# Kernel tuning notes

Hardware: AMD Instinct MI355X
Metric: run time of the kernel (lower is better)

The kernel has to match this reference:

```python
import jax, jax.numpy as jnp
import numpy as np

B_GRAPHS = 256
N_PER = 512
N = B_GRAPHS * N_PER            # 131072 nodes
E = 1048576                     # edges (avg degree 8)
H = 64                          # hidden_dim
L = 3                           # num_layers
R = 128                         # rnn_dim
NODE_IN = 2
EDGE_IN = 2
OUT = 2
JK = L * H


def setup_inputs() -> dict:
    key = jax.random.key(0)
    ks = jax.random.split(key, 40)
    # intra-graph random edges
    g = jax.random.randint(ks[0], (E,), 0, B_GRAPHS)
    src = g * N_PER + jax.random.randint(ks[1], (E,), 0, N_PER)
    dst = g * N_PER + jax.random.randint(ks[2], (E,), 0, N_PER)
    edge_index = jnp.stack([src, dst]).astype(jnp.int64)
    batch = jnp.repeat(jnp.arange(B_GRAPHS, dtype=jnp.int64), N_PER)

    p = lambda k, shp: jax.random.normal(k, shp, jnp.float32) * 0.1
    return dict(
        x=jax.random.normal(ks[3], (N, NODE_IN), jnp.float32),
        edge_attr=jax.random.normal(ks[4], (E, EDGE_IN), jnp.float32),
        node_W=p(ks[5], (NODE_IN, H)), node_b=p(ks[6], (H,)),
        edgeemb_W=p(ks[7], (EDGE_IN, H)), edgeemb_b=p(ks[8], (H,)),
        gat_W=p(ks[9], (L, H, H)), gat_Wedge=p(ks[10], (L, H, H)),
        gat_att_src=p(ks[11], (L, H)), gat_att_dst=p(ks[12], (L, H)),
        gat_att_edge=p(ks[13], (L, H)), gat_b=p(ks[14], (L, H)),
        gru_wih_f=p(ks[15], (3 * R, JK)), gru_whh_f=p(ks[16], (3 * R, R)),
        gru_bih_f=p(ks[17], (3 * R,)), gru_bhh_f=p(ks[18], (3 * R,)),
        gru_wih_b=p(ks[19], (3 * R, JK)), gru_whh_b=p(ks[20], (3 * R, R)),
        gru_bih_b=p(ks[21], (3 * R,)), gru_bhh_b=p(ks[22], (3 * R,)),
        head_W1=p(ks[23], (2 * R, 64)), head_b1=p(ks[24], (64,)),
        head_W2=p(ks[25], (64, OUT)), head_b2=p(ks[26], (OUT,)),
        edge_index=edge_index, batch=batch,
    )


def _gru_dir(xs, wih, whh, bih, bhh):
    # xs: [T, B, F] -> outputs [T, B, R]  (PyTorch GRU cell equations)
    gx = xs @ wih.T + bih  # precompute input gates [T, B, 3R]
    h0 = jnp.zeros((xs.shape[1], R), xs.dtype)

    def step(h, g):
        gh = h @ whh.T + bhh
        r = jax.nn.sigmoid(g[..., :R] + gh[..., :R])
        z = jax.nn.sigmoid(g[..., R:2 * R] + gh[..., R:2 * R])
        n = jnp.tanh(g[..., 2 * R:] + r * gh[..., 2 * R:])
        hn = (1.0 - z) * n + z * h
        return hn, hn

    _, ys = jax.lax.scan(step, h0, gx)
    return ys


def _forward(x, edge_attr, node_W, node_b, edgeemb_W, edgeemb_b,
             gat_W, gat_Wedge, gat_att_src, gat_att_dst, gat_att_edge, gat_b,
             gru_wih_f, gru_whh_f, gru_bih_f, gru_bhh_f,
             gru_wih_b, gru_whh_b, gru_bih_b, gru_bhh_b,
             head_W1, head_b1, head_W2, head_b2, edge_index, batch):
    src, dst = edge_index[0], edge_index[1]
    h = x @ node_W + node_b                     # [N, H]
    e = edge_attr @ edgeemb_W + edgeemb_b       # [E, H]

    # PyG GATConv default add_self_loops=True, fill_value='mean':
    # self-loop edge feature = mean of incoming edge features per node
    ones = jnp.ones((E,), e.dtype)
    deg = jax.ops.segment_sum(ones, dst, num_segments=N)
    e_loop = jax.ops.segment_sum(e, dst, num_segments=N) / jnp.maximum(deg, 1.0)[:, None]
    ar = jnp.arange(N, dtype=src.dtype)
    srcF = jnp.concatenate([src, ar])
    dstF = jnp.concatenate([dst, ar])
    eF = jnp.concatenate([e, e_loop], axis=0)   # [E+N, H]

    outs = []
    for l in range(L):
        xp = h @ gat_W[l]                                   # [N, H]
        a_s = xp @ gat_att_src[l]                           # [N]
        a_d = xp @ gat_att_dst[l]                           # [N]
        a_e = (eF @ gat_Wedge[l]) @ gat_att_edge[l]         # [E+N]
        alpha = jax.nn.leaky_relu(a_s[srcF] + a_d[dstF] + a_e, 0.2)
        m = jax.ops.segment_max(alpha, dstF, num_segments=N)
        ex = jnp.exp(alpha - m[dstF])
        den = jax.ops.segment_sum(ex, dstF, num_segments=N)
        w = ex / den[dstF]                                  # segment softmax
        agg = jax.ops.segment_sum(w[:, None] * xp[srcF], dstF, num_segments=N) + gat_b[l]
        h = jax.nn.leaky_relu(agg, 0.01)                    # F.leaky_relu default slope
        outs.append(h)

    h_jk = jnp.concatenate(outs, axis=-1)                   # [N, JK]
    # to_dense_batch: sorted equal-size graphs -> dense reshape, mask all True
    dense = h_jk.reshape(B_GRAPHS, N_PER, JK)
    xs = dense.transpose(1, 0, 2)                           # [T, B, JK]
    yf = _gru_dir(xs, gru_wih_f, gru_whh_f, gru_bih_f, gru_bhh_f)
    yb = _gru_dir(xs[::-1], gru_wih_b, gru_whh_b, gru_bih_b, gru_bhh_b)[::-1]
    rnn_out = jnp.concatenate([yf, yb], axis=-1).transpose(1, 0, 2)  # [B, T, 2R]
    out = jax.nn.relu(rnn_out @ head_W1 + head_b1) @ head_W2 + head_b2
    return out.reshape(N, OUT)                              # out[mask], mask full


def reference(x, edge_attr, node_W, node_b, edgeemb_W, edgeemb_b,
              gat_W, gat_Wedge, gat_att_src, gat_att_dst, gat_att_edge, gat_b,
              gru_wih_f, gru_whh_f, gru_bih_f, gru_bhh_f,
              gru_wih_b, gru_whh_b, gru_bih_b, gru_bhh_b,
              head_W1, head_b1, head_W2, head_b2, edge_index, batch):
    return _forward(x, edge_attr, node_W, node_b, edgeemb_W, edgeemb_b,
                    gat_W, gat_Wedge, gat_att_src, gat_att_dst, gat_att_edge, gat_b,
                    gru_wih_f, gru_whh_f, gru_bih_f, gru_bhh_f,
                    gru_wih_b, gru_whh_b, gru_bih_b, gru_bhh_b,
                    head_W1, head_b1, head_W2, head_b2, edge_index, batch)
```

## Files before the change

### kernel.cpp

```cpp
#include <hip/hip_runtime.h>
#include <cstdint>
#include <cstddef>

typedef _Float16 half_t;
typedef _Float16 half8 __attribute__((ext_vector_type(8)));
typedef float f32x4 __attribute__((ext_vector_type(4)));

constexpr int NN = 131072;
constexpr int NE = 1048576;
constexpr int NPER = 512;

#define DEVINL __device__ __forceinline__

DEVINL float sigm_(float x){ float e = __expf(-x); return __builtin_amdgcn_rcpf(1.f+e); }
DEVINL float tanh_(float x){
  x = fminf(15.f, fmaxf(-15.f, x));
  float e = __expf(-2.f*x);
  return (1.f-e)*__builtin_amdgcn_rcpf(1.f+e);
}

#define LDS_BARRIER() asm volatile("s_waitcnt lgkmcnt(0)\ns_barrier" ::: "memory")


__global__ void const_kernel(const float* __restrict__ gatWe,
                             const float* __restrict__ attE, const float* __restrict__ eW,
                             const float* __restrict__ eb, float* __restrict__ cc){
  int l = blockIdx.x, k = threadIdx.x;
  const float* Wel = gatWe + l*4096;
  float s3=0.f;
  for (int j=0;j<64;j++) s3 += Wel[k*64+j]*attE[l*64+j];
  float c0 = eW[k]*s3, c1 = eW[64+k]*s3, cb = eb[k]*s3;
  for (int off=1; off<64; off<<=1){
    c0 += __shfl_xor(c0,off); c1 += __shfl_xor(c1,off); cb += __shfl_xor(cb,off);
  }
  if (k==0){ cc[l]=c0; cc[3+l]=c1; cc[6+l]=cb; }
}

__global__ void prep_pack(const float* __restrict__ wih_f, const float* __restrict__ wih_b,
                          const float* __restrict__ head_W1, const float* __restrict__ gat_W,
                          const float* __restrict__ bih_f, const float* __restrict__ bih_b,
                          const float* __restrict__ whh_f, const float* __restrict__ whh_b,
                          half_t* __restrict__ BcombT, half_t* __restrict__ W1T,
                          half_t* __restrict__ BTgat, float* __restrict__ bias_comb,
                          half_t* __restrict__ whh16){
  int gid = blockIdx.x*256 + threadIdx.x;
  if (gid < 147456){
    int j = gid/192, k = gid%192;
    float v = (j<384)? wih_f[j*192+k] : wih_b[(j-384)*192+k];
    BcombT[gid] = (half_t)v;
  } else if (gid < 163840){
    int i = gid - 147456;
    int n = i>>8, k = i&255;
    W1T[i] = (half_t)head_W1[k*64+n];
  } else if (gid < 176128){
    int i = gid - 163840;
    int l = i>>12, r = i&4095;
    int n = r>>6, k = r&63;
    BTgat[i] = (half_t)gat_W[l*4096 + k*64 + n];
  } else if (gid < 176896){
    int i = gid - 176128;
    int j = (i<384)? i : i-384;
    bias_comb[i] = (i<384)? bih_f[j] : bih_b[j];
  } else if (gid < 275200){
    int i = gid - 176896;
    float v = (i<49152)? whh_f[i] : whh_b[i-49152];
    whh16[i] = (half_t)v;
  }
}

__global__ void bias_fold(const float* __restrict__ bhh_f, const float* __restrict__ bhh_b,
                          float* __restrict__ bias_comb){
  int i = threadIdx.x + blockIdx.x*256;
  if (i < 256)      bias_comb[i]       += bhh_f[i];
  else if (i < 512) bias_comb[i+128]   += bhh_b[i-256];
}

__global__ __launch_bounds__(256) void embed_kernel(const float* __restrict__ x,
                            const float* __restrict__ nW, const float* __restrict__ nb,
                            half_t* __restrict__ h){
  int gid = blockIdx.x*256 + threadIdx.x;
  int n = gid>>6, j = gid&63;
  float v = x[2*n]*nW[j] + x[2*n+1]*nW[64+j] + nb[j];
  h[(size_t)n*64+j] = (half_t)v;
}

__global__ __launch_bounds__(256) void deg_count(const int* __restrict__ ei,
                          int* __restrict__ deg, int* __restrict__ tmp){
  int e = blockIdx.x*256 + threadIdx.x;
  int dt = ei[NE+e];
  tmp[e] = atomicAdd(&deg[dt],1);
}

__global__ __launch_bounds__(256) void scan1(const int* __restrict__ deg, int* __restrict__ rowstart,
                      int* __restrict__ bsum){
  __shared__ int sc[256];
  int b=blockIdx.x, t=threadIdx.x, i=b*256+t;
  int v=deg[i]; sc[t]=v; __syncthreads();
  for (int off=1; off<256; off<<=1){
    int tv = (t>=off)? sc[t-off] : 0;
    __syncthreads(); sc[t]+=tv; __syncthreads();
  }
  rowstart[i]=sc[t]-v;
  if (t==255) bsum[b]=sc[255];
}
__global__ void scan2(int* __restrict__ bsum){
  __shared__ int sc[512];
  int t=threadIdx.x; int v=bsum[t]; sc[t]=v; __syncthreads();
  for (int off=1; off<512; off<<=1){
    int tv = (t>=off)? sc[t-off] : 0;
    __syncthreads(); sc[t]+=tv; __syncthreads();
  }
  bsum[t]=sc[t]-v;
}
__global__ __launch_bounds__(256) void scan3(int* __restrict__ rowstart, const int* __restrict__ bsum){
  int b=blockIdx.x, t=threadIdx.x, i=b*256+t;
  rowstart[i]+=bsum[b];
}

__global__ __launch_bounds__(256) void fill2(const int* __restrict__ ei, const float* __restrict__ ea,
                      const int* __restrict__ rowstart, const int* __restrict__ tmp,
                      int4* __restrict__ rec){
  int e = blockIdx.x*256 + threadIdx.x;
  int dt = ei[NE+e];
  int slot = rowstart[dt] + tmp[e];
  int4 r;
  r.x = ei[e];
  r.y = __float_as_int(ea[2*e]);
  r.z = __float_as_int(ea[2*e+1]);
  r.w = dt;
  rec[slot] = r;
}

__global__ __launch_bounds__(256) void means_kernel(const int* __restrict__ deg, const int* __restrict__ rowstart,
                         const int4* __restrict__ rec, float2* __restrict__ m01){
  int n = blockIdx.x*256 + threadIdx.x;
  int st = rowstart[n], cnt = deg[n];
  float s0=0.f, s1=0.f;
  for (int i=0;i<cnt;i++){
    int4 r = rec[st+i];
    s0 += __int_as_float(r.y);
    s1 += __int_as_float(r.z);
  }
  float inv = 1.f/(float)max(cnt,1);
  float2 m; m.x = s0*inv; m.y = s1*inv;
  m01[n] = m;
}

__global__ __launch_bounds__(256) void gemm_xp(const half_t* __restrict__ A, int lda,
                        const half_t* __restrict__ BT,
                        const float* __restrict__ attS, const float* __restrict__ attD,
                        half_t* __restrict__ xp, float* __restrict__ a_s, float* __restrict__ a_d){
  __shared__ half_t As[128*32];
  __shared__ half_t Bs[64*32];
  const int tid = threadIdx.x, m0 = blockIdx.x*128;
  const int w = tid>>6, lane = tid&63;
  const int lm = lane&15, quad = lane>>4;
  const int wm0 = w*32;
  f32x4 acc[2][4] = {};
  for (int k0=0;k0<64;k0+=32){
    {
      const int c0 = tid*2;
      #pragma unroll
      for (int u=0;u<2;u++){
        int c=c0+u; int row=c>>2; int off=(c&3)*8;
        *(half8*)(&As[row*32+off]) = *(const half8*)(&A[(size_t)(m0+row)*lda + k0 + off]);
      }
      int c=tid; int row=c>>2; int off=(c&3)*8;
      *(half8*)(&Bs[row*32+off]) = *(const half8*)(&BT[(size_t)row*64 + k0 + off]);
    }
    __syncthreads();
    half8 af[2], bf[4];
    #pragma unroll
    for (int nt=0;nt<4;nt++) bf[nt] = *(const half8*)(&Bs[(nt*16+lm)*32 + quad*8]);
    #pragma unroll
    for (int mt=0;mt<2;mt++) af[mt] = *(const half8*)(&As[(wm0+mt*16+lm)*32 + quad*8]);
    #pragma unroll
    for (int mt=0;mt<2;mt++)
      #pragma unroll
      for (int nt=0;nt<4;nt++)
        acc[mt][nt] = __builtin_amdgcn_mfma_f32_16x16x32_f16(af[mt], bf[nt], acc[mt][nt], 0,0,0);
    __syncthreads();
  }
  float vsv[4], vdv[4];
  #pragma unroll
  for (int nt=0;nt<4;nt++){ vsv[nt]=attS[nt*16+lm]; vdv[nt]=attD[nt*16+lm]; }
  #pragma unroll
  for (int mt=0;mt<2;mt++)
   #pragma unroll
   for (int r=0;r<4;r++){
    int m = m0+wm0+mt*16+quad*4+r;
    float ps=0.f, pd=0.f;
    #pragma unroll
    for (int nt=0;nt<4;nt++){
      float v = acc[mt][nt][r];
      xp[(size_t)m*64 + nt*16+lm] = (half_t)v;
      ps += v*vsv[nt]; pd += v*vdv[nt];
    }
    ps += __shfl_xor(ps,1); ps += __shfl_xor(ps,2); ps += __shfl_xor(ps,4); ps += __shfl_xor(ps,8);
    pd += __shfl_xor(pd,1); pd += __shfl_xor(pd,2); pd += __shfl_xor(pd,4); pd += __shfl_xor(pd,8);
    if (lm==0){ a_s[m]=ps; a_d[m]=pd; }
  }
}

__global__ __launch_bounds__(256) void edge_w(const int4* __restrict__ rec,
                       const float* __restrict__ a_s, const float* __restrict__ a_d,
                       const float* __restrict__ cc, int l, int2* __restrict__ sw,
                       const int* __restrict__ deg, const float2* __restrict__ m01,
                       float* __restrict__ wsf){
  int b = blockIdx.x;
  if (b < 4096){
    int s = b*256 + threadIdx.x;
    int4 r = rec[s];
    float al = a_s[r.x] + a_d[r.w]
             + __int_as_float(r.y)*cc[l] + __int_as_float(r.z)*cc[3+l] + cc[6+l];
    al = al>0.f? al : 0.2f*al;
    int2 o; o.x = r.x; o.y = __float_as_int(__expf(al));
    sw[s] = o;
  } else {
    int n = (b-4096)*256 + threadIdx.x;
    int cnt = deg[n];
    float2 m = m01[n];
    float ael = cnt? (m.x*cc[l] + m.y*cc[3+l] + cc[6+l]) : 0.f;
    float asl = a_s[n] + a_d[n] + ael;
    asl = asl>0.f? asl : 0.2f*asl;
    wsf[n] = __expf(asl);
  }
}

constexpr int SWCAP = 1536;
__global__ __launch_bounds__(512,4) void agg_lds(const int* __restrict__ rowstart, const int* __restrict__ deg,
                          const int2* __restrict__ sw, const float* __restrict__ wsf, int l,
                          const half_t* __restrict__ xp, const float* __restrict__ bias,
                          half_t* __restrict__ hjk){
  __shared__ half_t xs[512*64];
  __shared__ int2  swl[SWCAP];
  __shared__ int   nst[128];
  __shared__ int   ncnt[128];
  __shared__ float nwsf[128];
  const int g = blockIdx.x >> 2;
  const int sub = blockIdx.x & 3;
  const int tid = threadIdx.x;
  const int nbase = g*512 + sub*128;
  const int segst = rowstart[nbase];
  const int segend = rowstart[nbase+127] + deg[nbase+127];
  const int segcnt = segend - segst;
  {
    const half8* srcp = (const half8*)(xp + (size_t)g*32768);
    half8* dstp = (half8*)xs;
    #pragma unroll
    for (int i=0;i<8;i++)
      dstp[tid + i*512] = srcp[tid + i*512];
    int scap = segcnt < SWCAP ? segcnt : SWCAP;
    for (int i=tid; i<scap; i+=512)
      swl[i] = sw[segst+i];
    if (tid < 128){
      int n = nbase + tid;
      nst[tid]  = rowstart[n] - segst;
      ncnt[tid] = deg[n];
      nwsf[tid] = wsf[n];
    }
  }
  __syncthreads();
  const int w = tid>>6, lane = tid&63;
  const float bv = bias[lane];
  const int nb2 = nbase + w*16;
  for (int i=0;i<16;i++){
    const int li = w*16 + i;
    int st = nst[li], cnt = ncnt[li];
    float acc=0.f, den=0.f;
    if (cnt>0){
      if (st + cnt <= SWCAP){
        int q = cnt>>2, rem = cnt&3;
        int L0=q+(rem>0), L1=q+(rem>1), L2=q+(rem>2), L3=q;
        int s1v=L0, s2v=L0+L1, s3v=s2v+L2;
        int2 p0={0,0},p1={0,0},p2={0,0},p3={0,0};
        float x0v=0.f,x1v=0.f,x2v=0.f,x3v=0.f;
        if (L0>0){ p0=swl[st];     x0v=(float)xs[(p0.x&511)*64+lane]; }
        if (L1>0){ p1=swl[st+s1v]; x1v=(float)xs[(p1.x&511)*64+lane]; }
        if (L2>0){ p2=swl[st+s2v]; x2v=(float)xs[(p2.x&511)*64+lane]; }
        if (L3>0){ p3=swl[st+s3v]; x3v=(float)xs[(p3.x&511)*64+lane]; }
        for (int k=0;k<L0;k++){
          int2 n0=p0,n1=p1,n2=p2,n3=p3;
          float y0=0.f,y1=0.f,y2=0.f,y3=0.f;
          if (k+1<L0){ n0=swl[st+k+1];     y0=(float)xs[(n0.x&511)*64+lane]; }
          if (k+1<L1){ n1=swl[st+s1v+k+1]; y1=(float)xs[(n1.x&511)*64+lane]; }
          if (k+1<L2){ n2=swl[st+s2v+k+1]; y2=(float)xs[(n2.x&511)*64+lane]; }
          if (k+1<L3){ n3=swl[st+s3v+k+1]; y3=(float)xs[(n3.x&511)*64+lane]; }
          { float ww=__int_as_float(p0.y); den+=ww; acc+=ww*x0v; }
          if (k<L1){ float ww=__int_as_float(p1.y); den+=ww; acc+=ww*x1v; }
          if (k<L2){ float ww=__int_as_float(p2.y); den+=ww; acc+=ww*x2v; }
          if (k<L3){ float ww=__int_as_float(p3.y); den+=ww; acc+=ww*x3v; }
          p0=n0;p1=n1;p2=n2;p3=n3;
          x0v=y0;x1v=y1;x2v=y2;x3v=y3;
        }
      } else {
        int2 p = sw[segst+st];
        float xv = (float)xs[(p.x&511)*64 + lane];
        for (int k=0;k<cnt;k++){
          int2 pn = p; float xvn=0.f;
          if (k+1<cnt){
            pn = sw[segst+st+k+1];
            xvn = (float)xs[(pn.x&511)*64 + lane];
          }
          float ww = __int_as_float(p.y);
          den += ww;
          acc += ww*xv;
          p = pn; xv = xvn;
        }
      }
    }
    float wsfv = nwsf[li];
    den += wsfv;
    acc += wsfv*(float)xs[((nb2+i)&511)*64 + lane];
    float v = acc/den + bv;
    v = v>0.f? v : 0.01f*v;
    hjk[(size_t)(nb2+i)*192 + l*64 + lane] = (half_t)v;
  }
}

__global__ __launch_bounds__(256) void gemm_head(const half_t* __restrict__ A,
                        const half_t* __restrict__ W1T, const float* __restrict__ b1,
                        const float* __restrict__ W2, const float* __restrict__ b2,
                        float* __restrict__ out){
  __shared__ half_t As[128*32];
  __shared__ half_t Bs[64*32];
  const int tid = threadIdx.x, m0 = blockIdx.x*128;
  const int w = tid>>6, lane = tid&63;
  const int lm = lane&15, quad = lane>>4;
  const int wm0 = w*32;
  f32x4 acc[2][4] = {};
  for (int k0=0;k0<256;k0+=32){
    {
      const int c0 = tid*2;
      #pragma unroll
      for (int u=0;u<2;u++){
        int c=c0+u; int row=c>>2; int off=(c&3)*8;
        *(half8*)(&As[row*32+off]) = *(const half8*)(&A[(size_t)(m0+row)*256 + k0 + off]);
      }
      int c=tid; int row=c>>2; int off=(c&3)*8;
      *(half8*)(&Bs[row*32+off]) = *(const half8*)(&W1T[(size_t)row*256 + k0 + off]);
    }
    __syncthreads();
    half8 af[2], bf[4];
    #pragma unroll
    for (int nt=0;nt<4;nt++) bf[nt] = *(const half8*)(&Bs[(nt*16+lm)*32 + quad*8]);
    #pragma unroll
    for (int mt=0;mt<2;mt++) af[mt] = *(const half8*)(&As[(wm0+mt*16+lm)*32 + quad*8]);
    #pragma unroll
    for (int mt=0;mt<2;mt++)
      #pragma unroll
      for (int nt=0;nt<4;nt++)
        acc[mt][nt] = __builtin_amdgcn_mfma_f32_16x16x32_f16(af[mt], bf[nt], acc[mt][nt], 0,0,0);
    __syncthreads();
  }
  float b1v[4], w20[4], w21[4];
  #pragma unroll
  for (int nt=0;nt<4;nt++){
    int n = nt*16+lm;
    b1v[nt]=b1[n]; w20[nt]=W2[n*2]; w21[nt]=W2[n*2+1];
  }
  float b20=b2[0], b21=b2[1];
  #pragma unroll
  for (int mt=0;mt<2;mt++)
   #pragma unroll
   for (int r=0;r<4;r++){
    int m = m0+wm0+mt*16+quad*4+r;
    float p0=0.f, p1=0.f;
    #pragma unroll
    for (int nt=0;nt<4;nt++){
      float v = acc[mt][nt][r] + b1v[nt];
      v = v>0.f? v : 0.f;
      p0 += v*w20[nt]; p1 += v*w21[nt];
    }
    p0 += __shfl_xor(p0,1); p0 += __shfl_xor(p0,2); p0 += __shfl_xor(p0,4); p0 += __shfl_xor(p0,8);
    p1 += __shfl_xor(p1,1); p1 += __shfl_xor(p1,2); p1 += __shfl_xor(p1,4); p1 += __shfl_xor(p1,8);
    if (lm==0){
      out[(size_t)m*2]   = p0 + b20;
      out[(size_t)m*2+1] = p1 + b21;
    }
  }
}

__global__ __launch_bounds__(512,1) void gru_fused(
    const half_t* __restrict__ whh16, const float* __restrict__ bhh_f, const float* __restrict__ bhh_b,
    const half_t* __restrict__ gxf, const half_t* __restrict__ gxb,
    float* __restrict__ hstate, half_t* __restrict__ y, int c, int gruBlocks,
    const half_t* __restrict__ hjk, const half_t* __restrict__ BcombT, const float* __restrict__ biasc,
    half_t* __restrict__ gxf_n, half_t* __restrict__ gxb_n, int s0f, int s0b){
  __shared__ __align__(16) char SMEM[16384];
  const int bid = blockIdx.x;
  const int tid = threadIdx.x;
  if (bid < gruBlocks){
    __builtin_amdgcn_s_setprio(1);
    auto& H = *(half_t (*)[2][16][132])SMEM;
    half_t* slab0 = (half_t*)(SMEM + 8448);
    half_t* slab1 = (half_t*)(SMEM + 8448 + 3072);

    const int d = bid >> 6, gblk = bid & 63;
    const half_t* __restrict__ gx = d ? gxb : gxf;
    const float* bhh = d ? bhh_b : bhh_f;
    const int w = tid >> 6, lane = tid & 63;
    const int l15 = lane & 15, quad = lane >> 4;
    const int unit = w*16 + l15;

    half8 bf[3][4];
    float bhn = bhh[256 + unit];
    {
      const half_t* wbase = whh16 + (size_t)d*49152;
      #pragma unroll
      for (int g=0; g<3; g++){
        const half_t* wp = wbase + (size_t)(g*128 + unit)*128;
        #pragma unroll
        for (int kk=0; kk<4; kk++)
          bf[g][kk] = *(const half8*)(wp + kk*32 + quad*8);
      }
    }

    float hreg = hstate[((size_t)d*256 + gblk*4 + quad)*128 + unit];

    const bool loader = (w >= 4 && w < 7);
    const int jsl = d ? -384 : 384;
    int idx8 = 0;
    const half_t* srcp = nullptr;
    if (loader){
      int idx = (w-4)*64 + lane;
      int g_loc = idx/48, o = idx - g_loc*48;
      idx8 = idx*8;
      int j0 = d ? 127 : 0;
      srcp = gx + ((size_t)(gblk*4 + g_loc)*128 + j0)*384 + o*8;
    }

    const int cgg = tid >> 6;
    const int cpart = (tid & 63)*2;
    const int pos0 = d ? (511 - c*128) : (c*128);
    const int ystep = d ? -256 : 256;
    half_t* yptr = y + ((size_t)(gblk*4 + cgg)*512 + pos0)*256 + d*128 + cpart;

    for (int i=tid; i<2112; i+=512) ((uint*)SMEM)[i] = 0;
    LDS_BARRIER();
    H[0][quad*4][unit] = (half_t)hreg;
    half8 lvA, lvB;
    if (loader){
      lvA = *(const half8*)srcp; srcp += jsl;
      *(half8*)(slab0 + idx8) = lvA;
      lvB = *(const half8*)srcp; srcp += jsl;
    }
    LDS_BARRIER();

    auto stepf = [&](const half_t* cs, half_t* ns, int rd, int wr2,
                     half8& lvI, half8& lvW, bool pfi, bool pfw, bool cp){
      if (loader && pfi){ lvI = *(const half8*)srcp; srcp += jsl; }
      if (cp && tid < 256){
        uint hv = *(const uint*)&H[rd][cgg*4][cpart];
        *(uint*)yptr = hv;
        yptr += ystep;
      }
      float g0 = (float)cs[quad*384 + unit];
      float g1 = (float)cs[quad*384 + 128 + unit];
      float g2 = (float)cs[quad*384 + 256 + unit];
      half8 af[4] = {};
      if ((l15 & 3) == 0){
        #pragma unroll
        for (int kk=0; kk<4; kk++)
          af[kk] = *(const half8*)&H[rd][l15][kk*32 + quad*8];
      }
      f32x4 P[3] = {};
      #pragma unroll
      for (int kk=0; kk<4; kk++)
        #pragma unroll
        for (int g=0; g<3; g++)
          P[g] = __builtin_amdgcn_mfma_f32_16x16x32_f16(af[kk], bf[g][kk], P[g], 0,0,0);
      float rr = sigm_(g0 + P[0][0]);
      float zz = sigm_(g1 + P[1][0]);
      float nn = tanh_(g2 + rr*(P[2][0] + bhn));
      float hn = nn + zz*(hreg - nn);
      hreg = hn;
      H[wr2][quad*4][unit] = (half_t)hn;
      if (loader && pfw) *(half8*)(ns + idx8) = lvW;
      LDS_BARRIER();
    };

    stepf(slab0, slab1, 0,1, lvA, lvB, true,  true,  false);
    stepf(slab1, slab0, 1,0, lvB, lvA, true,  true,  true);
    for (int it=1; it<63; it++){
      stepf(slab0, slab1, 0,1, lvA, lvB, true, true, true);
      stepf(slab1, slab0, 1,0, lvB, lvA, true, true, true);
    }
    stepf(slab0, slab1, 0,1, lvA, lvB, false, true,  true);
    stepf(slab1, slab0, 1,0, lvB, lvA, false, false, true);
    if (tid < 256){
      uint hv = *(const uint*)&H[0][cgg*4][cpart];
      *(uint*)yptr = hv;
    }
    __builtin_amdgcn_s_setprio(0);
    hstate[((size_t)d*256 + gblk*4 + quad)*128 + unit] = hreg;
  } else {
    half_t* As = (half_t*)SMEM;
    half_t* Bs = (half_t*)(SMEM + 8192);
    const int gb = bid - gruBlocks;
    const int bx = gb & 255, by = gb >> 8;
    const int m0 = bx*128;
    const bool back = by >= 3;
    const int n0 = (back ? by-3 : by)*128;
    const int step0 = back ? s0b : s0f;
    half_t* C = back ? gxb_n : gxf_n;
    const half_t* BTh = BcombT + (back ? (size_t)384*192 : 0);
    const float* bh = biasc + (back ? 384 : 0);
    const int w = tid>>6, lane = tid&63;
    const int lm = lane&15, quad = lane>>4;
    const int wm0 = (w>>2)*64, wn0 = (w&3)*32;
    f32x4 acc[4][2] = {};
    for (int k0=0; k0<192; k0+=32){
      {
        int cidx = tid; int row = cidx>>2; int off = (cidx&3)*8;
        int m = m0+row;
        size_t arow = (size_t)(m>>7)*512 + step0 + (m&127);
        *(half8*)(&As[row*32+off]) = *(const half8*)(&hjk[arow*192 + k0 + off]);
        *(half8*)(&Bs[row*32+off]) = *(const half8*)(&BTh[(size_t)(n0+row)*192 + k0 + off]);
      }
      __syncthreads();
      half8 af[4], bfr[2];
      #pragma unroll
      for (int nt=0;nt<2;nt++) bfr[nt] = *(const half8*)(&Bs[(wn0+nt*16+lm)*32 + quad*8]);
      #pragma unroll
      for (int mt=0;mt<4;mt++) af[mt] = *(const half8*)(&As[(wm0+mt*16+lm)*32 + quad*8]);
      #pragma unroll
      for (int mt=0;mt<4;mt++)
        #pragma unroll
        for (int nt=0;nt<2;nt++)
          acc[mt][nt] = __builtin_amdgcn_mfma_f32_16x16x32_f16(af[mt], bfr[nt], acc[mt][nt], 0,0,0);
      __syncthreads();
    }
    #pragma unroll
    for (int mt=0;mt<4;mt++)
     #pragma unroll
     for (int nt=0;nt<2;nt++)
      #pragma unroll
      for (int r=0;r<4;r++){
        int m = m0+wm0+mt*16+quad*4+r;
        int n = n0+wn0+nt*16+lm;
        float v = acc[mt][nt][r] + bh[n];
        C[(size_t)m*384 + n] = (half_t)v;
      }
  }
}

extern "C" void kernel_launch(void* const* d_in, const int* in_sizes, int n_in,
                              void* d_out, int out_size, void* d_ws, size_t ws_size,
                              hipStream_t stream) {
  const float* x       = (const float*)d_in[0];
  const float* ea      = (const float*)d_in[1];
  const float* node_W  = (const float*)d_in[2];
  const float* node_b  = (const float*)d_in[3];
  const float* eW      = (const float*)d_in[4];
  const float* eb      = (const float*)d_in[5];
  const float* gat_W   = (const float*)d_in[6];
  const float* gat_We  = (const float*)d_in[7];
  const float* attS    = (const float*)d_in[8];
  const float* attD    = (const float*)d_in[9];
  const float* attE    = (const float*)d_in[10];
  const float* gat_b   = (const float*)d_in[11];
  const float* wih_f   = (const float*)d_in[12];
  const float* whh_f   = (const float*)d_in[13];
  const float* bih_f   = (const float*)d_in[14];
  const float* bhh_f   = (const float*)d_in[15];
  const float* wih_b   = (const float*)d_in[16];
  const float* whh_b   = (const float*)d_in[17];
  const float* bih_b   = (const float*)d_in[18];
  const float* bhh_b   = (const float*)d_in[19];
  const float* head_W1 = (const float*)d_in[20];
  const float* head_b1 = (const float*)d_in[21];
  const float* head_W2 = (const float*)d_in[22];
  const float* head_b2 = (const float*)d_in[23];
  const int*   ei      = (const int*)d_in[24];
  float* out = (float*)d_out;
  char* ws = (char*)d_ws;
  (void)in_sizes; (void)n_in; (void)out_size; (void)ws_size;

  size_t o = 0;
  auto alloc = [&](size_t bytes)->size_t{ size_t r=o; o += (bytes+255)&~(size_t)255; return r; };
  size_t o_cc     = alloc(16*4);
  size_t o_biasc  = alloc(768*4);
  size_t o_BcombT = alloc((size_t)768*192*2);
  size_t o_BTgat  = alloc((size_t)3*4096*2);
  size_t o_W1T    = alloc((size_t)64*256*2);
  size_t o_whh16  = alloc((size_t)2*49152*2);
  size_t o_hstate = alloc((size_t)2*256*128*4);
  size_t shared_base = o;

  size_t o_deg    = alloc((size_t)NN*4);
  size_t zero_end = o;
  size_t o_tmp    = alloc((size_t)NE*4);
  size_t o_rows   = alloc((size_t)NN*4);
  size_t o_bsum   = alloc(512*4);
  size_t o_rec    = alloc((size_t)NE*16);
  size_t o_sw     = alloc((size_t)NE*8);
  size_t o_m01    = alloc((size_t)NN*8);
  size_t o_as     = alloc((size_t)NN*4);
  size_t o_ad     = alloc((size_t)NN*4);
  size_t o_wsf    = alloc((size_t)NN*4);
  size_t o_h      = alloc((size_t)NN*64*2);
  size_t o_xp     = alloc((size_t)NN*64*2);
  size_t gat_end  = o;
  size_t gat_size = gat_end - shared_base;

  const size_t GXC    = (size_t)256*128*384*2;
  const size_t HJK_SZ = (size_t)NN*192*2;
  size_t shared_sz = gat_size > 4*GXC ? gat_size : 4*GXC;
  size_t o_gx0f = shared_base;
  size_t o_gx0b = shared_base + GXC;
  size_t o_gx1f = shared_base + 2*GXC;
  size_t o_gx1b = shared_base + 3*GXC;
  size_t o_hjk = shared_base + shared_sz;
  size_t o_y   = o_hjk + HJK_SZ;

  int*    deg    = (int*)(ws+o_deg);
  int*    tmp    = (int*)(ws+o_tmp);
  int*    rows   = (int*)(ws+o_rows);
  int*    bsum   = (int*)(ws+o_bsum);
  int4*   rec    = (int4*)(ws+o_rec);
  int2*   sw     = (int2*)(ws+o_sw);
  float2* m01    = (float2*)(ws+o_m01);
  float*  a_s    = (float*)(ws+o_as);
  float*  a_d    = (float*)(ws+o_ad);
  float*  wsf    = (float*)(ws+o_wsf);
  float*  cc     = (float*)(ws+o_cc);
  float*  biasc  = (float*)(ws+o_biasc);
  half_t* h      = (half_t*)(ws+o_h);
  half_t* xp     = (half_t*)(ws+o_xp);
  half_t* hjk    = (half_t*)(ws+o_hjk);
  half_t* BcombT = (half_t*)(ws+o_BcombT);
  half_t* BTgat  = (half_t*)(ws+o_BTgat);
  half_t* W1T    = (half_t*)(ws+o_W1T);
  half_t* whh16  = (half_t*)(ws+o_whh16);
  float*  hstate = (float*)(ws+o_hstate);
  half_t* gxbuf[2][2] = {{(half_t*)(ws+o_gx0f), (half_t*)(ws+o_gx0b)},
                         {(half_t*)(ws+o_gx1f), (half_t*)(ws+o_gx1b)}};
  half_t* y      = (half_t*)(ws+o_y);

  hipMemsetAsync(ws+shared_base, 0, zero_end-shared_base, stream);
  hipMemsetAsync(ws+o_hstate, 0, (size_t)2*256*128*4, stream);

  const_kernel<<<3,64,0,stream>>>(gat_We, attE, eW, eb, cc);
  prep_pack<<<1075,256,0,stream>>>(wih_f, wih_b, head_W1, gat_W, bih_f, bih_b, whh_f, whh_b,
                                   BcombT, W1T, BTgat, biasc, whh16);
  bias_fold<<<2,256,0,stream>>>(bhh_f, bhh_b, biasc);
  embed_kernel<<<32768,256,0,stream>>>(x, node_W, node_b, h);
  deg_count<<<4096,256,0,stream>>>(ei, deg, tmp);
  scan1<<<512,256,0,stream>>>(deg, rows, bsum);
  scan2<<<1,512,0,stream>>>(bsum);
  scan3<<<512,256,0,stream>>>(rows, bsum);
  fill2<<<4096,256,0,stream>>>(ei, ea, rows, tmp, rec);
  means_kernel<<<512,256,0,stream>>>(deg, rows, rec, m01);

  for (int l=0;l<3;l++){
    const half_t* in = (l==0)? h : (hjk + (size_t)(l-1)*64);
    int lda = (l==0)? 64 : 192;
    gemm_xp<<<1024,256,0,stream>>>(in, lda, BTgat + (size_t)l*4096, attS + l*64, attD + l*64, xp, a_s, a_d);
    edge_w<<<4608,256,0,stream>>>(rec, a_s, a_d, cc, l, sw, deg, m01, wsf);
    agg_lds<<<1024,512,0,stream>>>(rows, deg, sw, wsf, l, xp, gat_b + l*64, hjk);
  }

  gru_fused<<<1536,512,0,stream>>>(whh16, bhh_f, bhh_b, gxbuf[0][0], gxbuf[0][1], hstate, y, 0, 0,
                                   hjk, BcombT, biasc, gxbuf[0][0], gxbuf[0][1], 0, 384);
  for (int c=0;c<4;c++){
    int buf = c&1, nbuf = (c+1)&1;
    int grid = 128 + (c<3 ? 1536 : 0);
    gru_fused<<<grid,512,0,stream>>>(whh16, bhh_f, bhh_b, gxbuf[buf][0], gxbuf[buf][1], hstate, y, c, 128,
                                     hjk, BcombT, biasc, gxbuf[nbuf][0], gxbuf[nbuf][1],
                                     (c+1)*128, (2-c)*128);
  }

  gemm_head<<<1024,256,0,stream>>>(y, W1T, head_b1, head_W2, head_b2, out);
}
```

Before: 770.8 us.

## Aggregate GAT messages via LDS atomics instead of per-node gather from staged features

```diff
diff --git a/kernel.cpp b/kernel.cpp
--- a/kernel.cpp
+++ b/kernel.cpp
@@ -214,7 +214,9 @@
     float al = a_s[r.x] + a_d[r.w]
              + __int_as_float(r.y)*cc[l] + __int_as_float(r.z)*cc[3+l] + cc[6+l];
     al = al>0.f? al : 0.2f*al;
-    int2 o; o.x = r.x; o.y = __float_as_int(__expf(al));
+    int2 o;
+    o.x = (r.x & 511) | ((r.w & 127) << 16);
+    o.y = __float_as_int(__expf(al));
     sw[s] = o;
   } else {
     int n = (b-4096)*256 + threadIdx.x;
@@ -232,89 +234,57 @@
                           const int2* __restrict__ sw, const float* __restrict__ wsf, int l,
                           const half_t* __restrict__ xp, const float* __restrict__ bias,
                           half_t* __restrict__ hjk){
-  __shared__ half_t xs[512*64];
   __shared__ int2  swl[SWCAP];
-  __shared__ int   nst[128];
-  __shared__ int   ncnt[128];
-  __shared__ float nwsf[128];
-  const int g = blockIdx.x >> 2;
-  const int sub = blockIdx.x & 3;
+  __shared__ float accl[128*64];
+  __shared__ float denl[128];
   const int tid = threadIdx.x;
-  const int nbase = g*512 + sub*128;
+  const int nbase = blockIdx.x*128;
+  const half_t* __restrict__ xpg = xp + ((size_t)(nbase >> 9))*32768;
   const int segst = rowstart[nbase];
   const int segend = rowstart[nbase+127] + deg[nbase+127];
   const int segcnt = segend - segst;
-  {
-    const half8* srcp = (const half8*)(xp + (size_t)g*32768);
-    half8* dstp = (half8*)xs;
-    #pragma unroll
-    for (int i=0;i<8;i++)
-      dstp[tid + i*512] = srcp[tid + i*512];
-    int scap = segcnt < SWCAP ? segcnt : SWCAP;
-    for (int i=tid; i<scap; i+=512)
-      swl[i] = sw[segst+i];
-    if (tid < 128){
-      int n = nbase + tid;
-      nst[tid]  = rowstart[n] - segst;
-      ncnt[tid] = deg[n];
-      nwsf[tid] = wsf[n];
-    }
-  }
+  const int w = tid>>6, lane = tid&63;
+  #pragma unroll
+  for (int i=0;i<16;i++) accl[tid + i*512] = 0.f;
+  if (tid < 128) denl[tid] = 0.f;
+  int scap = segcnt < SWCAP ? segcnt : SWCAP;
+  for (int i=tid; i<scap; i+=512) swl[i] = sw[segst+i];
+  int e0 = rowstart[nbase + w*16] - segst;
+  int e1 = (w==7) ? segcnt : (rowstart[nbase + w*16 + 16] - segst);
   __syncthreads();
-  const int w = tid>>6, lane = tid&63;
+  if (segcnt <= SWCAP){
+    for (int e=e0; e<e1; ++e){
+      int2 p = swl[e];
+      int dl   = p.x >> 16;
+      int srcl = p.x & 511;
+      float xv = (float)xpg[(size_t)srcl*64 + lane];
+      float ww = __int_as_float(p.y);
+      atomicAdd(&accl[dl*64 + lane], ww*xv);
+      if (lane == 0) atomicAdd(&denl[dl], ww);
+    }
+  } else {
+    for (int e=e0; e<e1; ++e){
+      int2 p = sw[segst + e];
+      int dl   = p.x >> 16;
+      int srcl = p.x & 511;
+      float xv = (float)xpg[(size_t)srcl*64 + lane];
+      float ww = __int_as_float(p.y);
+      atomicAdd(&accl[dl*64 + lane], ww*xv);
+      if (lane == 0) atomicAdd(&denl[dl], ww);
+    }
+  }
+  __syncthreads();
   const float bv = bias[lane];
-  const int nb2 = nbase + w*16;
+  #pragma unroll
   for (int i=0;i<16;i++){
-    const int li = w*16 + i;
-    int st = nst[li], cnt = ncnt[li];
-    float acc=0.f, den=0.f;
-    if (cnt>0){
-      if (st + cnt <= SWCAP){
-        int q = cnt>>2, rem = cnt&3;
-        int L0=q+(rem>0), L1=q+(rem>1), L2=q+(rem>2), L3=q;
-        int s1v=L0, s2v=L0+L1, s3v=s2v+L2;
-        int2 p0={0,0},p1={0,0},p2={0,0},p3={0,0};
-        float x0v=0.f,x1v=0.f,x2v=0.f,x3v=0.f;
-        if (L0>0){ p0=swl[st];     x0v=(float)xs[(p0.x&511)*64+lane]; }
-        if (L1>0){ p1=swl[st+s1v]; x1v=(float)xs[(p1.x&511)*64+lane]; }
-        if (L2>0){ p2=swl[st+s2v]; x2v=(float)xs[(p2.x&511)*64+lane]; }
-        if (L3>0){ p3=swl[st+s3v]; x3v=(float)xs[(p3.x&511)*64+lane]; }
-        for (int k=0;k<L0;k++){
-          int2 n0=p0,n1=p1,n2=p2,n3=p3;
-          float y0=0.f,y1=0.f,y2=0.f,y3=0.f;
-          if (k+1<L0){ n0=swl[st+k+1];     y0=(float)xs[(n0.x&511)*64+lane]; }
-          if (k+1<L1){ n1=swl[st+s1v+k+1]; y1=(float)xs[(n1.x&511)*64+lane]; }
-          if (k+1<L2){ n2=swl[st+s2v+k+1]; y2=(float)xs[(n2.x&511)*64+lane]; }
-          if (k+1<L3){ n3=swl[st+s3v+k+1]; y3=(float)xs[(n3.x&511)*64+lane]; }
-          { float ww=__int_as_float(p0.y); den+=ww; acc+=ww*x0v; }
-          if (k<L1){ float ww=__int_as_float(p1.y); den+=ww; acc+=ww*x1v; }
-          if (k<L2){ float ww=__int_as_float(p2.y); den+=ww; acc+=ww*x2v; }
-          if (k<L3){ float ww=__int_as_float(p3.y); den+=ww; acc+=ww*x3v; }
-          p0=n0;p1=n1;p2=n2;p3=n3;
-          x0v=y0;x1v=y1;x2v=y2;x3v=y3;
-        }
-      } else {
-        int2 p = sw[segst+st];
-        float xv = (float)xs[(p.x&511)*64 + lane];
-        for (int k=0;k<cnt;k++){
-          int2 pn = p; float xvn=0.f;
-          if (k+1<cnt){
-            pn = sw[segst+st+k+1];
-            xvn = (float)xs[(pn.x&511)*64 + lane];
-          }
-          float ww = __int_as_float(p.y);
-          den += ww;
-          acc += ww*xv;
-          p = pn; xv = xvn;
-        }
-      }
-    }
-    float wsfv = nwsf[li];
-    den += wsfv;
-    acc += wsfv*(float)xs[((nb2+i)&511)*64 + lane];
-    float v = acc/den + bv;
+    int li = w*16 + i;
+    float accv = accl[li*64 + lane];
+    float den  = denl[li];
+    float wsfv = wsf[nbase + li];
+    float xv   = (float)xpg[(size_t)(((nbase+li)&511))*64 + lane];
+    float v = (accv + wsfv*xv)/(den + wsfv) + bv;
     v = v>0.f? v : 0.01f*v;
-    hjk[(size_t)(nb2+i)*192 + l*64 + lane] = (half_t)v;
+    hjk[(size_t)(nbase+li)*192 + l*64 + lane] = (half_t)v;
   }
 }
 
```

Result: slower. 1.691 ms (+119.4%).
